# Performance work log

Measured on AMD Instinct MI355X. Metric: run time of the kernel, lower is better.

## Reference

```python
import jax, jax.numpy as jnp
import numpy as np

B, T, D = 32, 1024, 384
T_OUT = 4096  # static padded output length (= target_len for every batch element)


def setup_inputs() -> dict:
    key = jax.random.key(0)
    k1, k2 = jax.random.split(key)
    x = jax.random.normal(k1, (B, T, D), dtype=jnp.float32)
    durations = jax.random.randint(k2, (B, T), 0, 8, dtype=jnp.int32)
    # constant target length -> torch pads/truncates every row to T_OUT,
    # and max over batch is T_OUT, so output is [B, T_OUT, D].
    target_len = jnp.full((B,), T_OUT, dtype=jnp.int32)
    return {"x": x, "durations": durations, "target_len": target_len}


def reference(x, durations, target_len):
    # x: [B, T, D]; durations: [B, T] int; target_len: [B] int.
    # Ragged repeat-expansion expressed as cumulative-duration searchsorted + gather.
    Bx, Tx, Dx = x.shape
    dur = jnp.maximum(durations, 0)
    ends = jnp.cumsum(dur, axis=1)              # [B, T] exclusive-end frame index per token
    total = ends[:, -1]                          # [B] total expanded length per batch row
    pos = jnp.arange(T_OUT, dtype=ends.dtype)    # [T_OUT] output frame positions
    # token index owning each output frame: number of ends <= pos
    idx = jax.vmap(lambda e: jnp.searchsorted(e, pos, side="right"))(ends)  # [B, T_OUT]
    idx = jnp.clip(idx, 0, Tx - 1)
    out = jnp.take_along_axis(x, idx[..., None], axis=1)  # [B, T_OUT, D]
    # frames past min(total_expansion, target_len) are zero padding (truncate + pad semantics)
    limit = jnp.minimum(total, target_len.astype(total.dtype))  # [B]
    valid = pos[None, :] < limit[:, None]                        # [B, T_OUT]
    return jnp.where(valid[..., None], out, jnp.zeros((), x.dtype))
```

## Files before the change

kernel.cpp:

```cpp
#include <hip/hip_runtime.h>


#define BB 32
#define TT 1024
#define DD 384
#define TOUT 4096
#define D4 (DD / 4)
#define N4 (TOUT * D4)

typedef float v4f __attribute__((ext_vector_type(4)));

__global__ __launch_bounds__(256) void lr_build_idx(
    const int4* __restrict__ dur4,
    const int* __restrict__ target_len,
    int* __restrict__ idx)
{
    __shared__ int ends[TT];
    __shared__ int sums[256];
    __shared__ int s_limit;
    const int b = blockIdx.x;
    const int q = threadIdx.x;

    int4 d = dur4[b * 256 + q];
    const int d0 = d.x > 0 ? d.x : 0;
    const int d1 = d.y > 0 ? d.y : 0;
    const int d2 = d.z > 0 ? d.z : 0;
    const int d3 = d.w > 0 ? d.w : 0;
    const int e0 = d0, e1 = e0 + d1, e2 = e1 + d2, e3 = e2 + d3;
    sums[q] = e3;
    __syncthreads();

    #pragma unroll
    for (int off = 1; off < 256; off <<= 1) {
        int u = (q >= off) ? sums[q - off] : 0;
        __syncthreads();
        sums[q] += u;
        __syncthreads();
    }
    const int base = sums[q] - e3;
    ((int4*)ends)[q] = make_int4(base + e0, base + e1, base + e2, base + e3);

    if (q == 255) {
        const int total = base + e3;
        const int tl = target_len[b];
        s_limit = total < tl ? total : tl;
    }
    __syncthreads();

    const int lim = s_limit;
    int lo[16];
    #pragma unroll
    for (int k = 0; k < 16; ++k) lo[k] = 0;
    #pragma unroll
    for (int s = 512; s > 0; s >>= 1) {
        #pragma unroll
        for (int k = 0; k < 16; ++k) {
            const int p = q + 256 * k;
            lo[k] += (ends[lo[k] + s - 1] <= p) ? s : 0;
        }
    }
    #pragma unroll
    for (int k = 0; k < 16; ++k) {
        const int p = q + 256 * k;
        int t = lo[k] > TT - 1 ? TT - 1 : lo[k];
        idx[b * TOUT + p] = (p < lim) ? t : -1;
    }
}

__global__ __launch_bounds__(256) void lr_gather(
    const v4f* __restrict__ x,
    const int* __restrict__ idx,
    v4f* __restrict__ out)
{
    const int b = blockIdx.y;
    const int base = blockIdx.x * 1024 + threadIdx.x;
    const int* __restrict__ idx_b = idx + b * TOUT;
    const v4f* __restrict__ x_b = x + b * TT * D4;
    v4f* __restrict__ out_b = out + b * N4;

    #pragma unroll
    for (int k = 0; k < 4; ++k) {
        const int i = base + k * 256;
        const int p = i / D4;
        const int c = i - p * D4;
        const int t = idx_b[p];
        v4f v = (v4f)(0.f);
        if (t >= 0) v = x_b[t * D4 + c];
        __builtin_nontemporal_store(v, out_b + i);
    }
}

extern "C" void kernel_launch(void* const* d_in, const int* in_sizes, int n_in,
                              void* d_out, int out_size, void* d_ws, size_t ws_size,
                              hipStream_t stream) {
    const float* x        = (const float*)d_in[0];
    const int* durations  = (const int*)d_in[1];
    const int* target_len = (const int*)d_in[2];
    float* out            = (float*)d_out;

    int* idx = (int*)d_ws;

    lr_build_idx<<<BB, 256, 0, stream>>>((const int4*)durations, target_len, idx);

    dim3 grid(N4 / 1024, BB);
    lr_gather<<<grid, 256, 0, stream>>>((const v4f*)x, idx, (v4f*)out);
}
```

Measured before the change: 245.5 us.

## Move searchsorted into gather blocks and drop the global index buffer

The first kernel now only computes the cumulative duration ends and the per-row limit. Each gather block loads the row's ends into shared memory and binary-searches the token index for just the roughly 24 output frames it covers. This spreads the search over many blocks instead of 32 and removes the intermediate idx array round trip. In exchange, every gather block reloads 4 KB of ends, runs a short serial search, and waits on two extra barriers. Each block now also handles twice as many elements.

```diff
diff --git a/kernel.cpp b/kernel.cpp
--- a/kernel.cpp
+++ b/kernel.cpp
@@ -7,17 +7,17 @@
 #define TOUT 4096
 #define D4 (DD / 4)
 #define N4 (TOUT * D4)
+#define EPB 2048
 
 typedef float v4f __attribute__((ext_vector_type(4)));
 
-__global__ __launch_bounds__(256) void lr_build_idx(
+__global__ __launch_bounds__(256) void lr_scan(
     const int4* __restrict__ dur4,
     const int* __restrict__ target_len,
-    int* __restrict__ idx)
+    int4* __restrict__ ends4,
+    int* __restrict__ limit)
 {
-    __shared__ int ends[TT];
     __shared__ int sums[256];
-    __shared__ int s_limit;
     const int b = blockIdx.x;
     const int q = threadIdx.x;
 
@@ -38,54 +38,54 @@
         __syncthreads();
     }
     const int base = sums[q] - e3;
-    ((int4*)ends)[q] = make_int4(base + e0, base + e1, base + e2, base + e3);
+    ends4[b * 256 + q] = make_int4(base + e0, base + e1, base + e2, base + e3);
 
     if (q == 255) {
         const int total = base + e3;
         const int tl = target_len[b];
-        s_limit = total < tl ? total : tl;
-    }
-    __syncthreads();
-
-    const int lim = s_limit;
-    int lo[16];
-    #pragma unroll
-    for (int k = 0; k < 16; ++k) lo[k] = 0;
-    #pragma unroll
-    for (int s = 512; s > 0; s >>= 1) {
-        #pragma unroll
-        for (int k = 0; k < 16; ++k) {
-            const int p = q + 256 * k;
-            lo[k] += (ends[lo[k] + s - 1] <= p) ? s : 0;
-        }
-    }
-    #pragma unroll
-    for (int k = 0; k < 16; ++k) {
-        const int p = q + 256 * k;
-        int t = lo[k] > TT - 1 ? TT - 1 : lo[k];
-        idx[b * TOUT + p] = (p < lim) ? t : -1;
+        limit[b] = total < tl ? total : tl;
     }
 }
 
 __global__ __launch_bounds__(256) void lr_gather(
     const v4f* __restrict__ x,
-    const int* __restrict__ idx,
+    const int4* __restrict__ ends4,
+    const int* __restrict__ limit,
     v4f* __restrict__ out)
 {
+    __shared__ int s_ends[TT];
+    __shared__ int s_trow[24];
     const int b = blockIdx.y;
-    const int base = blockIdx.x * 1024 + threadIdx.x;
-    const int* __restrict__ idx_b = idx + b * TOUT;
+    const int tid = threadIdx.x;
+    const int base0 = blockIdx.x * EPB;
+    const int p0 = base0 / D4;
+
+    ((int4*)s_ends)[tid] = ends4[b * 256 + tid];
+    const int lim = limit[b];
+    __syncthreads();
+
+    if (tid < 24) {
+        const int p = p0 + tid;
+        int lo = 0;
+        #pragma unroll
+        for (int s = 512; s > 0; s >>= 1) {
+            lo += (s_ends[lo + s - 1] <= p) ? s : 0;
+        }
+        s_trow[tid] = lo;
+    }
+    __syncthreads();
+
     const v4f* __restrict__ x_b = x + b * TT * D4;
     v4f* __restrict__ out_b = out + b * N4;
 
     #pragma unroll
-    for (int k = 0; k < 4; ++k) {
-        const int i = base + k * 256;
+    for (int k = 0; k < 8; ++k) {
+        const int i = base0 + k * 256 + tid;
         const int p = i / D4;
         const int c = i - p * D4;
-        const int t = idx_b[p];
+        const int t = s_trow[p - p0];
         v4f v = (v4f)(0.f);
-        if (t >= 0) v = x_b[t * D4 + c];
+        if (p < lim) v = x_b[t * D4 + c];
         __builtin_nontemporal_store(v, out_b + i);
     }
 }
@@ -98,10 +98,13 @@
     const int* target_len = (const int*)d_in[2];
     float* out            = (float*)d_out;
 
-    int* idx = (int*)d_ws;
+    int* limit = (int*)d_ws;
+    int* ends  = (int*)d_ws + 64;
 
-    lr_build_idx<<<BB, 256, 0, stream>>>((const int4*)durations, target_len, idx);
+    lr_scan<<<BB, 256, 0, stream>>>((const int4*)durations, target_len,
+                                    (int4*)ends, limit);
 
-    dim3 grid(N4 / 1024, BB);
-    lr_gather<<<grid, 256, 0, stream>>>((const v4f*)x, idx, (v4f*)out);
+    dim3 grid(N4 / EPB, BB);
+    lr_gather<<<grid, 256, 0, stream>>>((const v4f*)x, (const int4*)ends,
+                                        limit, (v4f*)out);
 }
```

Result: no change. 249.3 us (+1.6%).
